# Kernel optimization log

Measured on AMD Instinct MI355X. Metric: run time of the kernel, lower is better.

## Reference

```python
import math
import jax, jax.numpy as jnp
import numpy as np

D_MODEL = 1024
N_HEADS = 8
D_CONV = 4
D_INNER = 2 * D_MODEL
D_HIDDEN = 2 * D_MODEL
DH = D_INNER // N_HEADS
L = 2048
LN_EPS = 1e-5
GN_EPS = 1e-5
N_LAYERS = 12


def _layer_norm(x, w, eps=LN_EPS):
    m = jnp.mean(x, -1, keepdims=True)
    v = jnp.var(x, -1, keepdims=True)
    return (x - m) / jnp.sqrt(v + eps) * w


def _group_norm(h, w, b, eps=GN_EPS):
    # h: (L, D_INNER); N_HEADS groups of size DH
    hg = h.reshape(h.shape[0], N_HEADS, DH)
    m = jnp.mean(hg, -1, keepdims=True)
    v = jnp.var(hg, -1, keepdims=True)
    hn = ((hg - m) / jnp.sqrt(v + eps)).reshape(h.shape[0], D_INNER)
    return hn * w + b


def _mlstm(q, k, v, ig, fg, mask):
    # q,k,v: (nh, L, dh); ig,fg: (nh, L); mask: (L, L) bool causal
    nh, l, dh = q.shape
    log_fg_act = jax.nn.log_sigmoid(fg)
    cs = jnp.pad(jnp.cumsum(log_fg_act, -1), ((0, 0), (1, 0)))  # (nh, L+1)
    diff = cs[:, 1:, None] - cs[:, None, 1:]                    # (nh, L, L)
    log_fg_mat = jnp.where(mask, diff, -jnp.inf)
    log_D = log_fg_mat + ig[:, None, :]
    max_log_D = jnp.max(log_D, -1, keepdims=True)
    D = jnp.exp(log_D - max_log_D)
    scores = jnp.einsum('nld,nmd->nlm', q, k) / math.sqrt(dh)
    c = scores * D
    norm = jnp.maximum(jnp.abs(jnp.sum(c, -1, keepdims=True)), jnp.exp(-max_log_D))
    return jnp.einsum('nlm,nmd->nld', c / (norm + 1e-6), v)


def _forward(x, ln1_w, win_w, win_b, wout_w, conv_kernel, conv_bias, wq_w, wk_w, wv_w,
             igate_w, igate_b, fgate_w, fgate_b, gn_w, gn_b, skip, ln2_w,
             ffn_win_w, ffn_wout_w, mask):
    h = _layer_norm(x, ln1_w)
    # gated up-projection
    proj = h @ win_w.T + win_b                 # (L, 2*D_INNER)
    xi, res = proj[:, :D_INNER], proj[:, D_INNER:]
    # depthwise causal conv (jnp.convolve 'valid' semantics == correlate with flipped kernel)
    xp = jnp.pad(xi, ((D_CONV - 1, 0), (0, 0)))
    kf = conv_kernel[:, ::-1]
    windows = jnp.stack([xp[j:j + L] for j in range(D_CONV)], -1)  # (L, D_INNER, D_CONV)
    xc = jax.nn.silu(jnp.einsum('lcj,cj->lc', windows, kf) + conv_bias)

    def head_lin(z, w):
        # blockwise per-head linear: (L, nh, dh) x (nh, dh, dh)
        return jnp.einsum('lnh,nhd->lnd', z.reshape(L, N_HEADS, DH), w).reshape(L, D_INNER)

    q, k, v = head_lin(xc, wq_w), head_lin(xc, wk_w), head_lin(xi, wv_w)
    gate_in = jnp.concatenate([q, k, v], -1)   # (L, 3*D_INNER)
    ig = (gate_in @ igate_w.T + igate_b).T     # (nh, L)
    fg = (gate_in @ fgate_w.T + fgate_b).T     # (nh, L)
    to_heads = lambda z: z.reshape(L, N_HEADS, DH).transpose(1, 0, 2)
    hh = _mlstm(to_heads(q), to_heads(k), to_heads(v), ig, fg, mask)  # (nh, L, dh)
    h_flat = hh.transpose(1, 0, 2).reshape(L, D_INNER)
    h2 = _group_norm(h_flat, gn_w, gn_b) + skip * xc
    x = x + (h2 * jax.nn.silu(res)) @ wout_w.T
    # gated FFN
    hf = _layer_norm(x, ln2_w)
    p = hf @ ffn_win_w.T                        # (L, 2*D_HIDDEN)
    a, z = p[:, :D_HIDDEN], p[:, D_HIDDEN:]
    return x + (jax.nn.gelu(a) * z) @ ffn_wout_w.T


def setup_inputs() -> dict:
    key = jax.random.key(0)
    ks = jax.random.split(key, 12)
    small = lambda k, shape, dim: jax.random.normal(k, shape, dtype=jnp.float32) * math.sqrt(2.0 / (5.0 * dim))
    wang = lambda k, shape, dim: jax.random.normal(k, shape, dtype=jnp.float32) * (2.0 / (N_LAYERS * math.sqrt(dim)))
    return {
        'x': jax.random.normal(ks[0], (L, D_MODEL), dtype=jnp.float32),
        'mask': jnp.tril(jnp.ones((L, L), dtype=bool)),
        'ln1_w': jnp.ones(D_MODEL, jnp.float32),
        'win_w': small(ks[1], (2 * D_INNER, D_MODEL), D_MODEL),
        'win_b': jnp.zeros(2 * D_INNER, jnp.float32),
        'wout_w': wang(ks[2], (D_MODEL, D_INNER), D_INNER),
        'conv_kernel': small(ks[3], (D_INNER, D_CONV), D_INNER),
        'conv_bias': jnp.zeros(D_INNER, jnp.float32),
        'wq_w': small(ks[4], (N_HEADS, DH, DH), DH),
        'wk_w': small(ks[5], (N_HEADS, DH, DH), DH),
        'wv_w': small(ks[6], (N_HEADS, DH, DH), DH),
        'igate_w': small(ks[7], (N_HEADS, 3 * D_INNER), 3 * D_INNER),
        'igate_b': jnp.linspace(0.0, 0.1, N_HEADS, dtype=jnp.float32),
        'fgate_w': jnp.zeros((N_HEADS, 3 * D_INNER), jnp.float32),
        'fgate_b': jnp.linspace(3.0, 6.0, N_HEADS, dtype=jnp.float32),
        'gn_w': jnp.ones(D_INNER, jnp.float32),
        'gn_b': jnp.zeros(D_INNER, jnp.float32),
        'skip': jnp.ones(D_INNER, jnp.float32),
        'ln2_w': jnp.ones(D_MODEL, jnp.float32),
        'ffn_win_w': small(ks[8], (2 * D_HIDDEN, D_MODEL), D_MODEL),
        'ffn_wout_w': wang(ks[9], (D_MODEL, D_HIDDEN), D_HIDDEN),
    }


def reference(x, mask, ln1_w, win_w, win_b, wout_w, conv_kernel, conv_bias, wq_w, wk_w, wv_w,
              igate_w, igate_b, fgate_w, fgate_b, gn_w, gn_b, skip, ln2_w, ffn_win_w, ffn_wout_w):
    return _forward(x, ln1_w, win_w, win_b, wout_w, conv_kernel, conv_bias, wq_w, wk_w, wv_w,
                    igate_w, igate_b, fgate_w, fgate_b, gn_w, gn_b, skip, ln2_w,
                    ffn_win_w, ffn_wout_w, mask)
```

## Files before the change

### kernel.cpp

```cpp
#include <hip/hip_runtime.h>
#include <math.h>

#define L     2048
#define DM    1024
#define DI    2048
#define NH    8
#define DHD   256
#define DHID  2048

typedef short bf16x8 __attribute__((ext_vector_type(8)));
typedef float f32x4  __attribute__((ext_vector_type(4)));

__device__ inline float b2f(ushort h) {
  unsigned u = ((unsigned)h) << 16;
  return __builtin_bit_cast(float, u);
}
__device__ inline ushort f2b(float f) {
  unsigned u = __builtin_bit_cast(unsigned, f);
  unsigned r = (u + 0x7FFFu + ((u >> 16) & 1u)) >> 16;
  return (ushort)r;
}
__device__ inline unsigned pk2(ushort lo, ushort hi) { return (unsigned)lo | ((unsigned)hi << 16); }

__device__ inline bf16x8 frag_ld(const ushort* tile, int rowBytes, int row, int byte0) {
  const char* bp = (const char*)tile + row * rowBytes;
  const int sw = (row & 7) << 4;
  const int b1 = byte0 + 32;
  bf16x8 r;
  *(unsigned long long*)&r =
      *(const unsigned long long*)(bp + (((byte0 & ~15) ^ sw) | (byte0 & 15)));
  *((unsigned long long*)&r + 1) =
      *(const unsigned long long*)(bp + (((b1 & ~15) ^ sw) | (b1 & 15)));
  return r;
}

__global__ __launch_bounds__(256) void cast_kernel(const float* __restrict__ src,
    ushort* __restrict__ dst, int n) {
  const int i = (blockIdx.x * 256 + threadIdx.x) * 8;
  if (i >= n) return;
  float4 a = *(const float4*)(src + i);
  float4 b = *(const float4*)(src + i + 4);
  uint4 o;
  o.x = pk2(f2b(a.x), f2b(a.y));
  o.y = pk2(f2b(a.z), f2b(a.w));
  o.z = pk2(f2b(b.x), f2b(b.y));
  o.w = pk2(f2b(b.z), f2b(b.w));
  *(uint4*)(dst + i) = o;
}

__global__ __launch_bounds__(256) void wtrans_kernel(const float* __restrict__ wq,
    const float* __restrict__ wk, const float* __restrict__ wv, ushort* __restrict__ out) {
  const int z = blockIdx.z;
  const int mat = z >> 3, h = z & 7;
  const float* src = (mat == 0 ? wq : (mat == 1 ? wk : wv)) + (size_t)h * 65536;
  ushort* dst = out + (size_t)z * 65536;
  __shared__ float s[32][33];
  const int r = threadIdx.x >> 5, c = threadIdx.x & 31;
  const int I0 = blockIdx.y * 32, J0 = blockIdx.x * 32;
#pragma unroll
  for (int k = 0; k < 4; ++k) s[r + 8 * k][c] = src[(size_t)(I0 + r + 8 * k) * 256 + J0 + c];
  __syncthreads();
#pragma unroll
  for (int k = 0; k < 4; ++k)
    dst[(size_t)(J0 + r + 8 * k) * 256 + I0 + c] = f2b(s[c][r + 8 * k]);
}

__global__ __launch_bounds__(256) void ln_kernel(const float* __restrict__ x,
    const float* __restrict__ w, ushort* __restrict__ out, int D) {
  const int row = blockIdx.x;
  const float* xr = x + (size_t)row * D;
  const int i0 = threadIdx.x * 4;
  float4 v4 = *(const float4*)(xr + i0);
  float s  = v4.x + v4.y + v4.z + v4.w;
  float s2 = v4.x*v4.x + v4.y*v4.y + v4.z*v4.z + v4.w*v4.w;
#pragma unroll
  for (int off = 32; off; off >>= 1) { s += __shfl_xor(s, off); s2 += __shfl_xor(s2, off); }
  __shared__ float rs[4], rs2[4];
  if ((threadIdx.x & 63) == 0) { rs[threadIdx.x >> 6] = s; rs2[threadIdx.x >> 6] = s2; }
  __syncthreads();
  s  = rs[0] + rs[1] + rs[2] + rs[3];
  s2 = rs2[0] + rs2[1] + rs2[2] + rs2[3];
  const float mean = s / D;
  const float inv = rsqrtf(s2 / D - mean * mean + 1e-5f);
  float4 w4 = *(const float4*)(w + i0);
  ushort4 o4 = make_ushort4(
      f2b((v4.x - mean) * inv * w4.x), f2b((v4.y - mean) * inv * w4.y),
      f2b((v4.z - mean) * inv * w4.z), f2b((v4.w - mean) * inv * w4.w));
  *(ushort4*)(out + (size_t)row * D + i0) = o4;
}

template<bool BIAS, bool RESID, bool F32OUT, bool BF16OUT>
__global__ __launch_bounds__(256) void gemm_bf16(
    const ushort* __restrict__ A, int lda, long aBat,
    const ushort* __restrict__ B, int ldb, long bBat,
    const float* __restrict__ bias,
    const float* __restrict__ resid, int ldr,
    float* __restrict__ Cf, int ldc,
    ushort* __restrict__ Cb, int ldcb, int cbLim, long cBat,
    int K) {
  __shared__ ushort As[128 * 64];
  __shared__ ushort Bs[128 * 64];
  const int tid = threadIdx.x;
  const int w = tid >> 6, lane = tid & 63;
  const int g = lane >> 4, li = lane & 15;
  const int wr = (w >> 1) * 64, wc = (w & 1) * 64;
  const int row0 = blockIdx.y * 128, col0 = blockIdx.x * 128;
  const ushort* Ab = A + (size_t)blockIdx.z * aBat;
  const ushort* Bb = B + (size_t)blockIdx.z * bBat;

  f32x4 acc[4][4];
#pragma unroll
  for (int i = 0; i < 4; ++i)
#pragma unroll
    for (int j = 0; j < 4; ++j) acc[i][j] = (f32x4){0.f, 0.f, 0.f, 0.f};

  const int sr = tid >> 3;
  const int sb = tid & 7;
  const ushort* Ag = Ab + (size_t)(row0 + sr) * lda + sb * 8;
  const ushort* Bg = Bb + (size_t)(col0 + sr) * ldb + sb * 8;

  for (int k0 = 0; k0 < K; k0 += 64) {
    __syncthreads();
#pragma unroll
    for (int i = 0; i < 4; ++i) {
      const int r = sr + 32 * i;
      uint4 va = *(const uint4*)(Ag + (size_t)(32 * i) * lda + k0);
      uint4 vb = *(const uint4*)(Bg + (size_t)(32 * i) * ldb + k0);
      const int off = r * 128 + (((sb ^ (r & 7))) << 4);
      *(uint4*)((char*)As + off) = va;
      *(uint4*)((char*)Bs + off) = vb;
    }
    __syncthreads();
#pragma unroll
    for (int ks = 0; ks < 2; ++ks) {
      bf16x8 af[4], bfr[4];
      const int byte0 = ks * 64 + 8 * g;
#pragma unroll
      for (int rb = 0; rb < 4; ++rb) af[rb] = frag_ld(As, 128, wr + rb * 16 + li, byte0);
#pragma unroll
      for (int cb = 0; cb < 4; ++cb) bfr[cb] = frag_ld(Bs, 128, wc + cb * 16 + li, byte0);
#pragma unroll
      for (int rb = 0; rb < 4; ++rb)
#pragma unroll
        for (int cb = 0; cb < 4; ++cb)
          acc[rb][cb] = __builtin_amdgcn_mfma_f32_16x16x32_bf16(af[rb], bfr[cb], acc[rb][cb], 0, 0, 0);
    }
  }

#pragma unroll
  for (int rb = 0; rb < 4; ++rb)
#pragma unroll
    for (int cb = 0; cb < 4; ++cb)
#pragma unroll
      for (int j = 0; j < 4; ++j) {
        const int r = row0 + wr + rb * 16 + 4 * g + j;
        const int c = col0 + wc + cb * 16 + li;
        float v = acc[rb][cb][j];
        if (BIAS)  v += bias[c];
        if (RESID) v += resid[(size_t)r * ldr + c];
        if (F32OUT) Cf[(size_t)r * ldc + c] = v;
        if (BF16OUT) {
          if (c < cbLim) Cb[(size_t)blockIdx.z * cBat + (size_t)r * ldcb + c] = f2b(v);
        }
      }
}

__global__ __launch_bounds__(256) void conv_silu_kernel(const float* __restrict__ proj,
    const float* __restrict__ ck, const float* __restrict__ cb, ushort* __restrict__ xcb) {
  const int idx = blockIdx.x * 256 + threadIdx.x;
  const int l = idx >> 9, c4 = (idx & 511) * 4;
  float4 s = *(const float4*)(cb + c4);
#pragma unroll
  for (int t = 0; t < 4; ++t) {
    const int lm = l - t;
    if (lm >= 0) {
      float4 pv = *(const float4*)(proj + (size_t)lm * 4096 + c4);
      s.x = fmaf(ck[(c4 + 0) * 4 + t], pv.x, s.x);
      s.y = fmaf(ck[(c4 + 1) * 4 + t], pv.y, s.y);
      s.z = fmaf(ck[(c4 + 2) * 4 + t], pv.z, s.z);
      s.w = fmaf(ck[(c4 + 3) * 4 + t], pv.w, s.w);
    }
  }
  ushort4 o = make_ushort4(f2b(s.x / (1.f + __expf(-s.x))), f2b(s.y / (1.f + __expf(-s.y))),
                           f2b(s.z / (1.f + __expf(-s.z))), f2b(s.w / (1.f + __expf(-s.w))));
  *(ushort4*)(xcb + (size_t)l * 2048 + c4) = o;
}

__global__ __launch_bounds__(256) void gates_kernel(const ushort* __restrict__ qkv3,
    const ushort* __restrict__ gw, const float* __restrict__ igb, const float* __restrict__ fgb,
    float* __restrict__ ig_t, float* __restrict__ fg_t) {
  const int l = blockIdx.x;
  const ushort* row = qkv3 + (size_t)l * 6144;
  __shared__ float red[4];
  float rf[24];
#pragma unroll
  for (int ch = 0; ch < 3; ++ch) {
    uint4 u = *(const uint4*)(row + (threadIdx.x + 256 * ch) * 8);
    rf[ch*8+0] = b2f((ushort)u.x); rf[ch*8+1] = b2f((ushort)(u.x >> 16));
    rf[ch*8+2] = b2f((ushort)u.y); rf[ch*8+3] = b2f((ushort)(u.y >> 16));
    rf[ch*8+4] = b2f((ushort)u.z); rf[ch*8+5] = b2f((ushort)(u.z >> 16));
    rf[ch*8+6] = b2f((ushort)u.w); rf[ch*8+7] = b2f((ushort)(u.w >> 16));
  }
  for (int o = 0; o < 16; ++o) {
    const ushort* wr_ = gw + (size_t)o * 6144;
    float s = 0.f;
#pragma unroll
    for (int ch = 0; ch < 3; ++ch) {
      uint4 u = *(const uint4*)(wr_ + (threadIdx.x + 256 * ch) * 8);
      s += rf[ch*8+0] * b2f((ushort)u.x) + rf[ch*8+1] * b2f((ushort)(u.x >> 16));
      s += rf[ch*8+2] * b2f((ushort)u.y) + rf[ch*8+3] * b2f((ushort)(u.y >> 16));
      s += rf[ch*8+4] * b2f((ushort)u.z) + rf[ch*8+5] * b2f((ushort)(u.z >> 16));
      s += rf[ch*8+6] * b2f((ushort)u.w) + rf[ch*8+7] * b2f((ushort)(u.w >> 16));
    }
#pragma unroll
    for (int off = 32; off; off >>= 1) s += __shfl_xor(s, off);
    if ((threadIdx.x & 63) == 0) red[threadIdx.x >> 6] = s;
    __syncthreads();
    if (threadIdx.x == 0) {
      const int n = o & 7;
      float tot = red[0] + red[1] + red[2] + red[3] + ((o >= 8) ? fgb[n] : igb[n]);
      ((o >= 8) ? fg_t : ig_t)[(size_t)n * L + l] = tot;
    }
    __syncthreads();
  }
}

__global__ __launch_bounds__(256) void scan_kernel(const float* __restrict__ ig_t,
    const float* __restrict__ fg_t, float* __restrict__ e_b, float* __restrict__ M_b,
    float* __restrict__ wv_b) {
  const int n = blockIdx.x, t = threadIdx.x;
  const int base = n * L + t * 8;
  __shared__ float ps[256], pm[256];
  float lc[8];
  float run = 0.f;
#pragma unroll
  for (int j = 0; j < 8; ++j) {
    float xg = fg_t[base + j];
    float ls = (xg >= 0.f) ? -log1pf(expf(-xg)) : (xg - log1pf(expf(xg)));
    run += ls; lc[j] = run;
  }
  ps[t] = run;
  __syncthreads();
  if (t == 0) { float r = 0.f; for (int i = 0; i < 256; ++i) { float v = ps[i]; ps[i] = r; r += v; } }
  __syncthreads();
  const float eoff = ps[t];
  float wl[8]; float rm = -3.4e38f;
#pragma unroll
  for (int j = 0; j < 8; ++j) {
    float e = eoff + lc[j];
    float wv = ig_t[base + j] - e;
    e_b[base + j] = e; wv_b[base + j] = wv;
    rm = fmaxf(rm, wv); wl[j] = rm;
  }
  pm[t] = rm;
  __syncthreads();
  if (t == 0) { float r = -3.4e38f; for (int i = 0; i < 256; ++i) { float v = pm[i]; pm[i] = r; r = fmaxf(r, v); } }
  __syncthreads();
  const float moff = pm[t];
#pragma unroll
  for (int j = 0; j < 8; ++j) M_b[base + j] = fmaxf(moff, wl[j]);
}

__global__ __launch_bounds__(256) void mlstm_attn(const ushort* __restrict__ qkv3,
    const float* __restrict__ e_b, const float* __restrict__ M_b,
    const float* __restrict__ wv_b, float* __restrict__ hflat) {
  const int n = blockIdx.y;
  const int bx = blockIdx.x;
  const int tid = threadIdx.x;
  const int w = tid >> 6, lane = tid & 63;
  const int g = lane >> 4, li = lane & 15;
  const int qr = (w & 1) * 16, dh2 = (w >> 1) * 128;

  __shared__ ushort Qs[32 * 256];
  __shared__ ushort Ks[32 * 256];
  __shared__ ushort Vt[256 * 36];
  __shared__ float wvs[32];
  __shared__ float scl[2][16];

  const int sr = tid >> 3;
  const int sbb = tid & 7;

  for (int pass = 0; pass < 2; ++pass) {
    const int qt = pass ? (63 - bx) : bx;
    const int q0 = qt * 32;
    __syncthreads();
    {
      const ushort* qsrc = qkv3 + (size_t)(q0 + sr) * 6144 + n * 256;
      char* qrow = (char*)Qs + sr * 512;
#pragma unroll
      for (int i = 0; i < 4; ++i) {
        const int b = sbb + 8 * i;
        uint4 u = *(const uint4*)(qsrc + b * 8);
        uint4 o;
        o.x = pk2(f2b(b2f((ushort)u.x) * 0.0625f), f2b(b2f((ushort)(u.x >> 16)) * 0.0625f));
        o.y = pk2(f2b(b2f((ushort)u.y) * 0.0625f), f2b(b2f((ushort)(u.y >> 16)) * 0.0625f));
        o.z = pk2(f2b(b2f((ushort)u.z) * 0.0625f), f2b(b2f((ushort)(u.z >> 16)) * 0.0625f));
        o.w = pk2(f2b(b2f((ushort)u.w) * 0.0625f), f2b(b2f((ushort)(u.w >> 16)) * 0.0625f));
        *(uint4*)(qrow + ((b ^ (sr & 7)) << 4)) = o;
      }
    }
    __syncthreads();

    bf16x8 qf[8];
#pragma unroll
    for (int dc = 0; dc < 8; ++dc) qf[dc] = frag_ld(Qs, 512, qr + li, dc * 64 + 8 * g);

    const int qg = q0 + qr + li;
    const float Mq = M_b[(size_t)n * L + qg];
    const float el = e_b[(size_t)n * L + qg];
    float rowsum = 0.f;
    f32x4 oacc[8];
#pragma unroll
    for (int db = 0; db < 8; ++db) oacc[db] = (f32x4){0.f, 0.f, 0.f, 0.f};

    const int nmt = qt + 1;
    for (int mt = 0; mt < nmt; ++mt) {
      const int m0 = mt * 32;
      __syncthreads();
      {
        const ushort* ksrc = qkv3 + (size_t)(m0 + sr) * 6144 + 2048 + n * 256;
        const ushort* vsrc = qkv3 + (size_t)(m0 + sr) * 6144 + 4096 + n * 256;
        char* krow = (char*)Ks + sr * 512;
#pragma unroll
        for (int i = 0; i < 4; ++i) {
          const int b = sbb + 8 * i;
          uint4 ku = *(const uint4*)(ksrc + b * 8);
          *(uint4*)(krow + ((b ^ (sr & 7)) << 4)) = ku;
          uint4 vu = *(const uint4*)(vsrc + b * 8);
          const int d0 = b * 8;
          ushort* vp = Vt + sr;
          vp[(d0 + 0) * 36] = (ushort)vu.x; vp[(d0 + 1) * 36] = (ushort)(vu.x >> 16);
          vp[(d0 + 2) * 36] = (ushort)vu.y; vp[(d0 + 3) * 36] = (ushort)(vu.y >> 16);
          vp[(d0 + 4) * 36] = (ushort)vu.z; vp[(d0 + 5) * 36] = (ushort)(vu.z >> 16);
          vp[(d0 + 6) * 36] = (ushort)vu.w; vp[(d0 + 7) * 36] = (ushort)(vu.w >> 16);
        }
        if (tid < 32) wvs[tid] = wv_b[(size_t)n * L + m0 + tid];
      }
      __syncthreads();

      f32x4 st0 = (f32x4){0.f, 0.f, 0.f, 0.f}, st1 = (f32x4){0.f, 0.f, 0.f, 0.f};
#pragma unroll
      for (int dc = 0; dc < 8; ++dc) {
        bf16x8 kf0 = frag_ld(Ks, 512, li, dc * 64 + 8 * g);
        bf16x8 kf1 = frag_ld(Ks, 512, 16 + li, dc * 64 + 8 * g);
        st0 = __builtin_amdgcn_mfma_f32_16x16x32_bf16(kf0, qf[dc], st0, 0, 0, 0);
        st1 = __builtin_amdgcn_mfma_f32_16x16x32_bf16(kf1, qf[dc], st1, 0, 0, 0);
      }

      bf16x8 pa;
#pragma unroll
      for (int j = 0; j < 8; ++j) {
        const int h = j >> 2;
        const int mrel = 4 * g + (j & 3) + 16 * h;
        const float s = h ? st1[j & 3] : st0[j & 3];
        const int mg = m0 + mrel;
        float p = (mg <= qg) ? s * __expf(wvs[mrel] - Mq) : 0.f;
        rowsum += p;
        pa[j] = (short)f2b(p);
      }

#pragma unroll
      for (int db = 0; db < 8; ++db) {
        const ushort* vb = Vt + (dh2 + db * 16 + li) * 36;
        bf16x8 vf;
        *(unsigned long long*)&vf = *(const unsigned long long*)(vb + 4 * g);
        *((unsigned long long*)&vf + 1) = *(const unsigned long long*)(vb + 4 * g + 16);
        oacc[db] = __builtin_amdgcn_mfma_f32_16x16x32_bf16(pa, vf, oacc[db], 0, 0, 0);
      }
    }

    rowsum += __shfl_xor(rowsum, 16);
    rowsum += __shfl_xor(rowsum, 32);
    const float sc = 1.f / (fmaxf(fabsf(rowsum), __expf(-(el + Mq))) + 1e-6f);
    if (w < 2 && lane < 16) scl[w][lane] = sc;
    __syncthreads();
    float scj[4];
#pragma unroll
    for (int j = 0; j < 4; ++j) scj[j] = scl[w & 1][4 * g + j];
#pragma unroll
    for (int db = 0; db < 8; ++db)
#pragma unroll
      for (int j = 0; j < 4; ++j)
        hflat[(size_t)(q0 + qr + 4 * g + j) * 2048 + n * 256 + dh2 + db * 16 + li] =
            oacc[db][j] * scj[j];
  }
}

__global__ __launch_bounds__(64) void gn_y_kernel(const float* __restrict__ hflat,
    const ushort* __restrict__ xcb, const float* __restrict__ proj,
    const float* __restrict__ gnw, const float* __restrict__ gnb,
    const float* __restrict__ skip, ushort* __restrict__ yb) {
  const int n = blockIdx.x, l = blockIdx.y, lane = threadIdx.x;
  const float* hr = hflat + (size_t)l * DI + n * DHD;
  float vals[4]; float s = 0.f, s2 = 0.f;
#pragma unroll
  for (int u = 0; u < 4; ++u) {
    float t = hr[lane + u * 64]; vals[u] = t; s += t; s2 += t * t;
  }
#pragma unroll
  for (int off = 32; off; off >>= 1) { s += __shfl_xor(s, off); s2 += __shfl_xor(s2, off); }
  const float mean = s * (1.f / DHD);
  const float inv = rsqrtf(s2 * (1.f / DHD) - mean * mean + 1e-5f);
#pragma unroll
  for (int u = 0; u < 4; ++u) {
    const int c = n * DHD + lane + u * 64;
    const float hn = (vals[u] - mean) * inv;
    const float h2 = hn * gnw[c] + gnb[c] + skip[c] * b2f(xcb[(size_t)l * DI + c]);
    const float r = proj[(size_t)l * 4096 + 2048 + c];
    yb[(size_t)l * DI + c] = f2b(h2 * (r / (1.f + __expf(-r))));
  }
}

__global__ __launch_bounds__(256) void gelu_mul_kernel(const float* __restrict__ p,
    ushort* __restrict__ gb) {
  const int idx = blockIdx.x * 256 + threadIdx.x;
  const int l = idx >> 9, c4 = (idx & 511) * 4;
  float4 a = *(const float4*)(p + (size_t)l * 4096 + c4);
  float4 z = *(const float4*)(p + (size_t)l * 4096 + 2048 + c4);
  float o[4];
  float av[4] = {a.x, a.y, a.z, a.w};
  float zv[4] = {z.x, z.y, z.z, z.w};
#pragma unroll
  for (int j = 0; j < 4; ++j) {
    const float t = 0.7978845608028654f * (av[j] + 0.044715f * av[j] * av[j] * av[j]);
    o[j] = 0.5f * av[j] * (1.f + tanhf(t)) * zv[j];
  }
  *(ushort4*)(gb + (size_t)l * 2048 + c4) =
      make_ushort4(f2b(o[0]), f2b(o[1]), f2b(o[2]), f2b(o[3]));
}

extern "C" void kernel_launch(void* const* d_in, const int* in_sizes, int n_in,
                              void* d_out, int out_size, void* d_ws, size_t ws_size,
                              hipStream_t stream) {
  const float* x     = (const float*)d_in[0];
  const float* ln1w  = (const float*)d_in[2];
  const float* winw  = (const float*)d_in[3];
  const float* winb  = (const float*)d_in[4];
  const float* woutw = (const float*)d_in[5];
  const float* ck    = (const float*)d_in[6];
  const float* cb    = (const float*)d_in[7];
  const float* wq    = (const float*)d_in[8];
  const float* wk    = (const float*)d_in[9];
  const float* wvw   = (const float*)d_in[10];
  const float* igw   = (const float*)d_in[11];
  const float* igb   = (const float*)d_in[12];
  const float* fgw   = (const float*)d_in[13];
  const float* fgb   = (const float*)d_in[14];
  const float* gnw   = (const float*)d_in[15];
  const float* gnb   = (const float*)d_in[16];
  const float* skip  = (const float*)d_in[17];
  const float* ln2w  = (const float*)d_in[18];
  const float* fwin  = (const float*)d_in[19];
  const float* fwout = (const float*)d_in[20];
  float* out = (float*)d_out;

  char* base = (char*)d_ws;
  const size_t MB = 1ull << 20;
  float*  proj  = (float*)(base);
  float*  hflat = (float*)(base + 32 * MB);
  float*  x2    = (float*)(base + 48 * MB);
  float*  ig_t  = (float*)(base + 56 * MB);
  float*  fg_t  = ig_t + NH * L;
  float*  e_b   = fg_t + NH * L;
  float*  M_b   = e_b + NH * L;
  float*  wv_b  = M_b + NH * L;
  ushort* hb    = (ushort*)(base + 57 * MB);
  ushort* projb = (ushort*)(base + 61 * MB);
  ushort* xcb   = (ushort*)(base + 69 * MB);
  ushort* qkv3  = (ushort*)(base + 77 * MB);
  ushort* wA    = (ushort*)(base + 101 * MB);
  ushort* wB    = (ushort*)(base + 109 * MB);
  ushort* wqkvT = (ushort*)(base + 113 * MB);
  ushort* gwB   = (ushort*)(base + 116 * MB);
  ushort* yb    = projb;
  ushort* gb    = projb;

  cast_kernel<<<2048, 256, 0, stream>>>(winw, wA, 4096 * 1024);
  cast_kernel<<<1024, 256, 0, stream>>>(woutw, wB, 1024 * 2048);
  wtrans_kernel<<<dim3(8, 8, 24), 256, 0, stream>>>(wq, wk, wvw, wqkvT);
  cast_kernel<<<24, 256, 0, stream>>>(igw, gwB, 8 * 6144);
  cast_kernel<<<24, 256, 0, stream>>>(fgw, gwB + 8 * 6144, 8 * 6144);

  ln_kernel<<<L, 256, 0, stream>>>(x, ln1w, hb, DM);
  gemm_bf16<true, false, true, true><<<dim3(32, 16, 1), 256, 0, stream>>>(
      hb, 1024, 0, wA, 1024, 0, winb, nullptr, 0, proj, 4096, projb, 2048, 2048, 0, 1024);
  conv_silu_kernel<<<(L * 512) / 256, 256, 0, stream>>>(proj, ck, cb, xcb);
  gemm_bf16<false, false, false, true><<<dim3(2, 16, 8), 256, 0, stream>>>(
      xcb, 2048, 256, wqkvT, 256, 65536, nullptr, nullptr, 0, nullptr, 0,
      qkv3, 6144, 1 << 30, 256, 256);
  gemm_bf16<false, false, false, true><<<dim3(2, 16, 8), 256, 0, stream>>>(
      xcb, 2048, 256, wqkvT + 8 * 65536, 256, 65536, nullptr, nullptr, 0, nullptr, 0,
      qkv3 + 2048, 6144, 1 << 30, 256, 256);
  gemm_bf16<false, false, false, true><<<dim3(2, 16, 8), 256, 0, stream>>>(
      projb, 2048, 256, wqkvT + 16 * 65536, 256, 65536, nullptr, nullptr, 0, nullptr, 0,
      qkv3 + 4096, 6144, 1 << 30, 256, 256);
  gates_kernel<<<L, 256, 0, stream>>>(qkv3, gwB, igb, fgb, ig_t, fg_t);
  scan_kernel<<<NH, 256, 0, stream>>>(ig_t, fg_t, e_b, M_b, wv_b);
  mlstm_attn<<<dim3(32, 8), 256, 0, stream>>>(qkv3, e_b, M_b, wv_b, hflat);
  gn_y_kernel<<<dim3(NH, L), 64, 0, stream>>>(hflat, xcb, proj, gnw, gnb, skip, yb);
  gemm_bf16<false, true, true, false><<<dim3(8, 16, 1), 256, 0, stream>>>(
      yb, 2048, 0, wB, 2048, 0, nullptr, x, 1024, x2, 1024, nullptr, 0, 0, 0, 2048);
  ln_kernel<<<L, 256, 0, stream>>>(x2, ln2w, hb, DM);
  cast_kernel<<<2048, 256, 0, stream>>>(fwin, wA, 4096 * 1024);
  cast_kernel<<<1024, 256, 0, stream>>>(fwout, wB, 1024 * 2048);
  gemm_bf16<false, false, true, false><<<dim3(32, 16, 1), 256, 0, stream>>>(
      hb, 1024, 0, wA, 1024, 0, nullptr, nullptr, 0, proj, 4096, nullptr, 0, 0, 0, 1024);
  gelu_mul_kernel<<<(L * 512) / 256, 256, 0, stream>>>(proj, gb);
  gemm_bf16<false, true, true, false><<<dim3(8, 16, 1), 256, 0, stream>>>(
      gb, 2048, 0, wB, 2048, 0, nullptr, x2, 1024, out, 1024, nullptr, 0, 0, 0, 2048);
}
```

Measured before the change: 590.2 us.

## Rework mLSTM attention with double-buffered async LDS loads and transposed reads

The GEMM tile loader now uses global_load_lds direct-to-LDS copies instead of register staging. The mLSTM attention kernel is restructured to 512 threads per block with one query tile per block, ordered longest-first. It double-buffers K/V tiles via async global-to-LDS loads and reads V through ds_read_b64_tr_b16 instead of a manual scalar transpose. The conv reads the bf16 projection copy instead of fp32, and the attention output is stored as bf16, which halves the traffic into the group-norm kernel. The Q scale moves into the exponent as -ln16. Together these cut staging overhead and memory traffic, at the cost of bf16 rounding of intermediates and reliance on gfx950-specific instructions.

```diff
diff --git a/kernel.cpp b/kernel.cpp
--- a/kernel.cpp
+++ b/kernel.cpp
@@ -9,6 +9,7 @@
 #define DHID  2048
 
 typedef short bf16x8 __attribute__((ext_vector_type(8)));
+typedef short s16x4  __attribute__((ext_vector_type(4)));
 typedef float f32x4  __attribute__((ext_vector_type(4)));
 
 __device__ inline float b2f(ushort h) {
@@ -21,6 +22,12 @@
   return (ushort)r;
 }
 __device__ inline unsigned pk2(ushort lo, ushort hi) { return (unsigned)lo | ((unsigned)hi << 16); }
+
+#define GLD16(gp, lp) __builtin_amdgcn_global_load_lds( \
+    (const __attribute__((address_space(1))) void*)(gp), \
+    (__attribute__((address_space(3))) void*)(lp), 16, 0, 0)
+
+#define LDS_OFF(p) ((unsigned)(unsigned long long)(const __attribute__((address_space(3))) void*)(p))
 
 __device__ inline bf16x8 frag_ld(const ushort* tile, int rowBytes, int row, int byte0) {
   const char* bp = (const char*)tile + row * rowBytes;
@@ -105,30 +112,24 @@
   const int g = lane >> 4, li = lane & 15;
   const int wr = (w >> 1) * 64, wc = (w & 1) * 64;
   const int row0 = blockIdx.y * 128, col0 = blockIdx.x * 128;
-  const ushort* Ab = A + (size_t)blockIdx.z * aBat;
-  const ushort* Bb = B + (size_t)blockIdx.z * bBat;
+  const ushort* Ab = A + (size_t)blockIdx.z * aBat + (size_t)row0 * lda;
+  const ushort* Bb = B + (size_t)blockIdx.z * bBat + (size_t)col0 * ldb;
 
   f32x4 acc[4][4];
 #pragma unroll
   for (int i = 0; i < 4; ++i)
 #pragma unroll
     for (int j = 0; j < 4; ++j) acc[i][j] = (f32x4){0.f, 0.f, 0.f, 0.f};
-
-  const int sr = tid >> 3;
-  const int sb = tid & 7;
-  const ushort* Ag = Ab + (size_t)(row0 + sr) * lda + sb * 8;
-  const ushort* Bg = Bb + (size_t)(col0 + sr) * ldb + sb * 8;
 
   for (int k0 = 0; k0 < K; k0 += 64) {
     __syncthreads();
 #pragma unroll
     for (int i = 0; i < 4; ++i) {
-      const int r = sr + 32 * i;
-      uint4 va = *(const uint4*)(Ag + (size_t)(32 * i) * lda + k0);
-      uint4 vb = *(const uint4*)(Bg + (size_t)(32 * i) * ldb + k0);
-      const int off = r * 128 + (((sb ^ (r & 7))) << 4);
-      *(uint4*)((char*)As + off) = va;
-      *(uint4*)((char*)Bs + off) = vb;
+      const int BB = w * 4 + i;
+      const int r = BB * 8 + (lane >> 3);
+      const int c = (lane & 7) ^ (r & 7);
+      GLD16(Ab + (size_t)r * lda + k0 + c * 8, (char*)As + BB * 1024);
+      GLD16(Bb + (size_t)r * ldb + k0 + c * 8, (char*)Bs + BB * 1024);
     }
     __syncthreads();
 #pragma unroll
@@ -165,7 +166,7 @@
       }
 }
 
-__global__ __launch_bounds__(256) void conv_silu_kernel(const float* __restrict__ proj,
+__global__ __launch_bounds__(256) void conv_silu_kernel(const ushort* __restrict__ xib,
     const float* __restrict__ ck, const float* __restrict__ cb, ushort* __restrict__ xcb) {
   const int idx = blockIdx.x * 256 + threadIdx.x;
   const int l = idx >> 9, c4 = (idx & 511) * 4;
@@ -174,11 +175,11 @@
   for (int t = 0; t < 4; ++t) {
     const int lm = l - t;
     if (lm >= 0) {
-      float4 pv = *(const float4*)(proj + (size_t)lm * 4096 + c4);
-      s.x = fmaf(ck[(c4 + 0) * 4 + t], pv.x, s.x);
-      s.y = fmaf(ck[(c4 + 1) * 4 + t], pv.y, s.y);
-      s.z = fmaf(ck[(c4 + 2) * 4 + t], pv.z, s.z);
-      s.w = fmaf(ck[(c4 + 3) * 4 + t], pv.w, s.w);
+      ushort4 pv = *(const ushort4*)(xib + (size_t)lm * 2048 + c4);
+      s.x = fmaf(ck[(c4 + 0) * 4 + t], b2f(pv.x), s.x);
+      s.y = fmaf(ck[(c4 + 1) * 4 + t], b2f(pv.y), s.y);
+      s.z = fmaf(ck[(c4 + 2) * 4 + t], b2f(pv.z), s.z);
+      s.w = fmaf(ck[(c4 + 3) * 4 + t], b2f(pv.w), s.w);
     }
   }
   ushort4 o = make_ushort4(f2b(s.x / (1.f + __expf(-s.x))), f2b(s.y / (1.f + __expf(-s.y))),
@@ -261,141 +262,146 @@
   for (int j = 0; j < 8; ++j) M_b[base + j] = fmaxf(moff, wl[j]);
 }
 
-__global__ __launch_bounds__(256) void mlstm_attn(const ushort* __restrict__ qkv3,
+__global__ __launch_bounds__(512, 4) void mlstm_attn(const ushort* __restrict__ qkv3,
     const float* __restrict__ e_b, const float* __restrict__ M_b,
-    const float* __restrict__ wv_b, float* __restrict__ hflat) {
-  const int n = blockIdx.y;
-  const int bx = blockIdx.x;
+    const float* __restrict__ wv_b, ushort* __restrict__ hflat) {
+  const int n = blockIdx.x & 7;
+  const int u = blockIdx.x >> 3;
+  const int qt = (u < 32) ? (63 - u) : (u - 32);
+  const int q0 = qt * 32;
   const int tid = threadIdx.x;
   const int w = tid >> 6, lane = tid & 63;
   const int g = lane >> 4, li = lane & 15;
-  const int qr = (w & 1) * 16, dh2 = (w >> 1) * 128;
-
-  __shared__ ushort Qs[32 * 256];
-  __shared__ ushort Ks[32 * 256];
-  __shared__ ushort Vt[256 * 36];
-  __shared__ float wvs[32];
-  __shared__ float scl[2][16];
-
-  const int sr = tid >> 3;
-  const int sbb = tid & 7;
-
-  for (int pass = 0; pass < 2; ++pass) {
-    const int qt = pass ? (63 - bx) : bx;
-    const int q0 = qt * 32;
+  const int qr = (w & 1) * 16, dq = (w >> 1) * 64;
+
+  __shared__ ushort Kb[2][32 * 256];
+  __shared__ ushort Vb[2][32 * 256];
+
+  const size_t headoff = (size_t)n * 256;
+  const ushort* kbase = qkv3 + 2048 + headoff;
+  const ushort* vbase = qkv3 + 4096 + headoff;
+
+#pragma unroll
+  for (int c = 0; c < 2; ++c) {
+    const int BB = w * 2 + c;
+    const int r = BB * 2 + (lane >> 5);
+    const int cc = (lane & 31) ^ (r & 7);
+    GLD16(qkv3 + (size_t)(q0 + r) * 6144 + headoff + cc * 8, (char*)Vb[0] + BB * 1024);
+  }
+  __syncthreads();
+  bf16x8 qf[8];
+#pragma unroll
+  for (int dc = 0; dc < 8; ++dc) qf[dc] = frag_ld(Vb[0], 512, qr + li, dc * 64 + 8 * g);
+  const int qg = q0 + qr + li;
+  const float Mq = M_b[(size_t)n * L + qg];
+  const float el = e_b[(size_t)n * L + qg];
+  __syncthreads();
+
+  auto stage_kv = [&](int m0, int buf) {
+#pragma unroll
+    for (int c = 0; c < 2; ++c) {
+      const int BB = w * 2 + c;
+      {
+        const int r = BB * 2 + (lane >> 5);
+        const int cc = (lane & 31) ^ (r & 7);
+        GLD16(kbase + (size_t)(m0 + r) * 6144 + cc * 8, (char*)Kb[buf] + BB * 1024);
+      }
+      {
+        const int BI = BB * 64 + lane;
+        const int m = ((BI >> 9) & 1) * 16 + ((BI >> 3) & 3) * 4 + ((BI >> 1) & 3);
+        const int d = ((BI >> 5) & 15) * 16 + (BI & 1) * 8;
+        GLD16(vbase + (size_t)(m0 + m) * 6144 + d, (char*)Vb[buf] + BB * 1024);
+      }
+    }
+  };
+
+  stage_kv(0, 0);
+
+  float rowsum = 0.f;
+  f32x4 oacc[4];
+#pragma unroll
+  for (int t = 0; t < 4; ++t) oacc[t] = (f32x4){0.f, 0.f, 0.f, 0.f};
+
+  const float LN16 = 2.772588722239781f;
+  const unsigned vcol = (unsigned)((dq >> 4) * 512 + g * 128 + li * 2);
+  const int nmt = qt + 1;
+
+  for (int mt = 0; mt < nmt; ++mt) {
     __syncthreads();
-    {
-      const ushort* qsrc = qkv3 + (size_t)(q0 + sr) * 6144 + n * 256;
-      char* qrow = (char*)Qs + sr * 512;
-#pragma unroll
-      for (int i = 0; i < 4; ++i) {
-        const int b = sbb + 8 * i;
-        uint4 u = *(const uint4*)(qsrc + b * 8);
-        uint4 o;
-        o.x = pk2(f2b(b2f((ushort)u.x) * 0.0625f), f2b(b2f((ushort)(u.x >> 16)) * 0.0625f));
-        o.y = pk2(f2b(b2f((ushort)u.y) * 0.0625f), f2b(b2f((ushort)(u.y >> 16)) * 0.0625f));
-        o.z = pk2(f2b(b2f((ushort)u.z) * 0.0625f), f2b(b2f((ushort)(u.z >> 16)) * 0.0625f));
-        o.w = pk2(f2b(b2f((ushort)u.w) * 0.0625f), f2b(b2f((ushort)(u.w >> 16)) * 0.0625f));
-        *(uint4*)(qrow + ((b ^ (sr & 7)) << 4)) = o;
-      }
-    }
-    __syncthreads();
-
-    bf16x8 qf[8];
-#pragma unroll
-    for (int dc = 0; dc < 8; ++dc) qf[dc] = frag_ld(Qs, 512, qr + li, dc * 64 + 8 * g);
-
-    const int qg = q0 + qr + li;
-    const float Mq = M_b[(size_t)n * L + qg];
-    const float el = e_b[(size_t)n * L + qg];
-    float rowsum = 0.f;
-    f32x4 oacc[8];
-#pragma unroll
-    for (int db = 0; db < 8; ++db) oacc[db] = (f32x4){0.f, 0.f, 0.f, 0.f};
-
-    const int nmt = qt + 1;
-    for (int mt = 0; mt < nmt; ++mt) {
-      const int m0 = mt * 32;
-      __syncthreads();
-      {
-        const ushort* ksrc = qkv3 + (size_t)(m0 + sr) * 6144 + 2048 + n * 256;
-        const ushort* vsrc = qkv3 + (size_t)(m0 + sr) * 6144 + 4096 + n * 256;
-        char* krow = (char*)Ks + sr * 512;
-#pragma unroll
-        for (int i = 0; i < 4; ++i) {
-          const int b = sbb + 8 * i;
-          uint4 ku = *(const uint4*)(ksrc + b * 8);
-          *(uint4*)(krow + ((b ^ (sr & 7)) << 4)) = ku;
-          uint4 vu = *(const uint4*)(vsrc + b * 8);
-          const int d0 = b * 8;
-          ushort* vp = Vt + sr;
-          vp[(d0 + 0) * 36] = (ushort)vu.x; vp[(d0 + 1) * 36] = (ushort)(vu.x >> 16);
-          vp[(d0 + 2) * 36] = (ushort)vu.y; vp[(d0 + 3) * 36] = (ushort)(vu.y >> 16);
-          vp[(d0 + 4) * 36] = (ushort)vu.z; vp[(d0 + 5) * 36] = (ushort)(vu.z >> 16);
-          vp[(d0 + 6) * 36] = (ushort)vu.w; vp[(d0 + 7) * 36] = (ushort)(vu.w >> 16);
-        }
-        if (tid < 32) wvs[tid] = wv_b[(size_t)n * L + m0 + tid];
-      }
-      __syncthreads();
-
-      f32x4 st0 = (f32x4){0.f, 0.f, 0.f, 0.f}, st1 = (f32x4){0.f, 0.f, 0.f, 0.f};
-#pragma unroll
-      for (int dc = 0; dc < 8; ++dc) {
-        bf16x8 kf0 = frag_ld(Ks, 512, li, dc * 64 + 8 * g);
-        bf16x8 kf1 = frag_ld(Ks, 512, 16 + li, dc * 64 + 8 * g);
-        st0 = __builtin_amdgcn_mfma_f32_16x16x32_bf16(kf0, qf[dc], st0, 0, 0, 0);
-        st1 = __builtin_amdgcn_mfma_f32_16x16x32_bf16(kf1, qf[dc], st1, 0, 0, 0);
-      }
-
-      bf16x8 pa;
-#pragma unroll
-      for (int j = 0; j < 8; ++j) {
-        const int h = j >> 2;
-        const int mrel = 4 * g + (j & 3) + 16 * h;
-        const float s = h ? st1[j & 3] : st0[j & 3];
-        const int mg = m0 + mrel;
-        float p = (mg <= qg) ? s * __expf(wvs[mrel] - Mq) : 0.f;
-        rowsum += p;
-        pa[j] = (short)f2b(p);
-      }
-
-#pragma unroll
-      for (int db = 0; db < 8; ++db) {
-        const ushort* vb = Vt + (dh2 + db * 16 + li) * 36;
-        bf16x8 vf;
-        *(unsigned long long*)&vf = *(const unsigned long long*)(vb + 4 * g);
-        *((unsigned long long*)&vf + 1) = *(const unsigned long long*)(vb + 4 * g + 16);
-        oacc[db] = __builtin_amdgcn_mfma_f32_16x16x32_bf16(pa, vf, oacc[db], 0, 0, 0);
-      }
-    }
-
-    rowsum += __shfl_xor(rowsum, 16);
-    rowsum += __shfl_xor(rowsum, 32);
-    const float sc = 1.f / (fmaxf(fabsf(rowsum), __expf(-(el + Mq))) + 1e-6f);
-    if (w < 2 && lane < 16) scl[w][lane] = sc;
-    __syncthreads();
-    float scj[4];
-#pragma unroll
-    for (int j = 0; j < 4; ++j) scj[j] = scl[w & 1][4 * g + j];
-#pragma unroll
-    for (int db = 0; db < 8; ++db)
-#pragma unroll
-      for (int j = 0; j < 4; ++j)
-        hflat[(size_t)(q0 + qr + 4 * g + j) * 2048 + n * 256 + dh2 + db * 16 + li] =
-            oacc[db][j] * scj[j];
-  }
-}
-
-__global__ __launch_bounds__(64) void gn_y_kernel(const float* __restrict__ hflat,
+    if (mt + 1 < nmt) stage_kv((mt + 1) * 32, (mt + 1) & 1);
+
+    const int m0 = mt * 32;
+    const int bsel = mt & 1;
+
+    const float4 wv0 = *(const float4*)(wv_b + (size_t)n * L + m0 + 4 * g);
+    const float4 wv1 = *(const float4*)(wv_b + (size_t)n * L + m0 + 16 + 4 * g);
+
+    f32x4 st0 = (f32x4){0.f, 0.f, 0.f, 0.f}, st1 = (f32x4){0.f, 0.f, 0.f, 0.f};
+#pragma unroll
+    for (int dc = 0; dc < 8; ++dc) {
+      bf16x8 kf0 = frag_ld(Kb[bsel], 512, li, dc * 64 + 8 * g);
+      bf16x8 kf1 = frag_ld(Kb[bsel], 512, 16 + li, dc * 64 + 8 * g);
+      st0 = __builtin_amdgcn_mfma_f32_16x16x32_bf16(kf0, qf[dc], st0, 0, 0, 0);
+      st1 = __builtin_amdgcn_mfma_f32_16x16x32_bf16(kf1, qf[dc], st1, 0, 0, 0);
+    }
+
+    s16x4 tr[8];
+    const unsigned vb0 = LDS_OFF((const char*)Vb[bsel]) + vcol;
+#pragma unroll
+    for (int t = 0; t < 4; ++t) {
+      const unsigned a0 = vb0 + t * 512;
+      asm volatile("ds_read_b64_tr_b16 %0, %1" : "=v"(tr[2 * t]) : "v"(a0));
+      asm volatile("ds_read_b64_tr_b16 %0, %1 offset:8192" : "=v"(tr[2 * t + 1]) : "v"(a0));
+    }
+
+    bf16x8 pa;
+#pragma unroll
+    for (int j = 0; j < 8; ++j) {
+      const int h = j >> 2;
+      const int mrel = 4 * g + (j & 3) + 16 * h;
+      const float s = h ? st1[j & 3] : st0[j & 3];
+      const float wvj = h ? ((const float*)&wv1)[j & 3] : ((const float*)&wv0)[j & 3];
+      float p = (m0 + mrel <= qg) ? s * __expf(wvj - Mq - LN16) : 0.f;
+      rowsum += p;
+      pa[j] = (short)f2b(p);
+    }
+
+    asm volatile("s_waitcnt lgkmcnt(0)" ::: "memory");
+    __builtin_amdgcn_sched_barrier(0);
+
+#pragma unroll
+    for (int t = 0; t < 4; ++t) {
+      bf16x8 vf;
+      vf[0] = tr[2*t][0]; vf[1] = tr[2*t][1]; vf[2] = tr[2*t][2]; vf[3] = tr[2*t][3];
+      vf[4] = tr[2*t+1][0]; vf[5] = tr[2*t+1][1]; vf[6] = tr[2*t+1][2]; vf[7] = tr[2*t+1][3];
+      oacc[t] = __builtin_amdgcn_mfma_f32_16x16x32_bf16(pa, vf, oacc[t], 0, 0, 0);
+    }
+  }
+
+  rowsum += __shfl_xor(rowsum, 16);
+  rowsum += __shfl_xor(rowsum, 32);
+  const float sc = 1.f / (fmaxf(fabsf(rowsum), __expf(-(el + Mq))) + 1e-6f);
+  float scj[4];
+#pragma unroll
+  for (int j = 0; j < 4; ++j) scj[j] = __shfl(sc, 4 * g + j);
+#pragma unroll
+  for (int t = 0; t < 4; ++t)
+#pragma unroll
+    for (int j = 0; j < 4; ++j)
+      hflat[(size_t)(q0 + qr + 4 * g + j) * 2048 + headoff + dq + t * 16 + li] =
+          f2b(oacc[t][j] * scj[j]);
+}
+
+__global__ __launch_bounds__(64) void gn_y_kernel(const ushort* __restrict__ hflat,
     const ushort* __restrict__ xcb, const float* __restrict__ proj,
     const float* __restrict__ gnw, const float* __restrict__ gnb,
     const float* __restrict__ skip, ushort* __restrict__ yb) {
   const int n = blockIdx.x, l = blockIdx.y, lane = threadIdx.x;
-  const float* hr = hflat + (size_t)l * DI + n * DHD;
+  const ushort* hr = hflat + (size_t)l * DI + n * DHD;
   float vals[4]; float s = 0.f, s2 = 0.f;
 #pragma unroll
   for (int u = 0; u < 4; ++u) {
-    float t = hr[lane + u * 64]; vals[u] = t; s += t; s2 += t * t;
+    float t = b2f(hr[lane + u * 64]); vals[u] = t; s += t; s2 += t * t;
   }
 #pragma unroll
   for (int off = 32; off; off >>= 1) { s += __shfl_xor(s, off); s2 += __shfl_xor(s2, off); }
@@ -457,7 +463,7 @@
   char* base = (char*)d_ws;
   const size_t MB = 1ull << 20;
   float*  proj  = (float*)(base);
-  float*  hflat = (float*)(base + 32 * MB);
+  ushort* hflat = (ushort*)(base + 32 * MB);
   float*  x2    = (float*)(base + 48 * MB);
   float*  ig_t  = (float*)(base + 56 * MB);
   float*  fg_t  = ig_t + NH * L;
@@ -484,7 +490,7 @@
   ln_kernel<<<L, 256, 0, stream>>>(x, ln1w, hb, DM);
   gemm_bf16<true, false, true, true><<<dim3(32, 16, 1), 256, 0, stream>>>(
       hb, 1024, 0, wA, 1024, 0, winb, nullptr, 0, proj, 4096, projb, 2048, 2048, 0, 1024);
-  conv_silu_kernel<<<(L * 512) / 256, 256, 0, stream>>>(proj, ck, cb, xcb);
+  conv_silu_kernel<<<(L * 512) / 256, 256, 0, stream>>>(projb, ck, cb, xcb);
   gemm_bf16<false, false, false, true><<<dim3(2, 16, 8), 256, 0, stream>>>(
       xcb, 2048, 256, wqkvT, 256, 65536, nullptr, nullptr, 0, nullptr, 0,
       qkv3, 6144, 1 << 30, 256, 256);
@@ -496,7 +502,7 @@
       qkv3 + 4096, 6144, 1 << 30, 256, 256);
   gates_kernel<<<L, 256, 0, stream>>>(qkv3, gwB, igb, fgb, ig_t, fg_t);
   scan_kernel<<<NH, 256, 0, stream>>>(ig_t, fg_t, e_b, M_b, wv_b);
-  mlstm_attn<<<dim3(32, 8), 256, 0, stream>>>(qkv3, e_b, M_b, wv_b, hflat);
+  mlstm_attn<<<512, 512, 0, stream>>>(qkv3, e_b, M_b, wv_b, hflat);
   gn_y_kernel<<<dim3(NH, L), 64, 0, stream>>>(hflat, xcb, proj, gnw, gnb, skip, yb);
   gemm_bf16<false, true, true, false><<<dim3(8, 16, 1), 256, 0, stream>>>(
       yb, 2048, 0, wB, 2048, 0, nullptr, x, 1024, x2, 1024, nullptr, 0, 0, 0, 2048);
```

Result: slower. 650.8 us (+10.3%).
